# Kernel tuning notes

Hardware: AMD Instinct MI355X
Metric: run time of the kernel (lower is better)

Reference implementation:

```python
import jax, jax.numpy as jnp
import numpy as np

DIM = 384
B = 256
EPS = 1e-5


def _conv_replicate(x, W, pad):
    # x: [B,C,H,W], W: [O,I,kh,kw]; replicate (edge) padding then VALID conv
    x = jnp.pad(x, ((0, 0), (0, 0), (pad, pad), (pad, pad)), mode='edge')
    return jax.lax.conv_general_dilated(
        x, W, window_strides=(1, 1), padding='VALID',
        dimension_numbers=('NCHW', 'OIHW', 'NCHW'))


def _bn(x, g, b, m, v):
    scale = (g / jnp.sqrt(v + EPS))[None, :, None, None]
    return (x - m[None, :, None, None]) * scale + b[None, :, None, None]


def _clip_features(target, bbox):
    # target: [B, 576, C] -> vectorized per-sample crop + nearest resize to 12x12
    bb = bbox * 24.0
    x, y, w, h = bb[:, 0], bb[:, 1], bb[:, 2], bb[:, 3]
    l = (w + h) / 2
    l = jnp.sqrt((w + l) * (h + l))
    x_min = jnp.clip(jnp.ceil(x - l / 2), 0, 23).astype(jnp.int32)
    y_min = jnp.clip(jnp.ceil(y - l / 2), 0, 23).astype(jnp.int32)
    x_max = jnp.clip(jnp.trunc(x + l / 2), 0, 23).astype(jnp.int32)
    y_max = jnp.clip(jnp.trunc(y + l / 2), 0, 23).astype(jnp.int32)
    i12 = jnp.arange(12, dtype=jnp.int32)
    # nearest-neighbor source index: crop_start + floor(i * crop_size / 12)
    rows = y_min[:, None] + (i12[None, :] * (y_max - y_min)[:, None]) // 12  # [B,12]
    cols = x_min[:, None] + (i12[None, :] * (x_max - x_min)[:, None]) // 12  # [B,12]
    rows = jnp.clip(rows, 0, 23)
    cols = jnp.clip(cols, 0, 23)
    Bn, N, C = target.shape
    tflat = jnp.transpose(target, (0, 2, 1))  # [B, C, 576] (row-major 24x24)
    idx = rows[:, :, None] * 24 + cols[:, None, :]  # [B,12,12]
    idx = jnp.broadcast_to(idx.reshape(Bn, 1, 144), (Bn, C, 144))
    out = jnp.take_along_axis(tflat, idx, axis=2)  # [B, C, 144]
    return out.reshape(Bn, C, 12, 12)


def setup_inputs() -> dict:
    key = jax.random.key(0)
    ks = jax.random.split(key, 8)
    temp = jax.random.normal(ks[0], (B, 144, DIM), dtype=jnp.float32)
    target = jax.random.normal(ks[1], (B, 576, DIM), dtype=jnp.float32)
    u = jax.random.uniform(ks[2], (B, 4), dtype=jnp.float32)
    # centers in [0.3,0.7], sizes in [0.25,0.45] -> always a valid non-empty crop
    bbox = jnp.concatenate([0.3 + 0.4 * u[:, :2], 0.25 + 0.2 * u[:, 2:]], axis=1)
    W1 = jax.random.normal(ks[3], (DIM, DIM, 5, 5), dtype=jnp.float32) * 0.02
    W2 = jax.random.normal(ks[4], (DIM, DIM, 3, 3), dtype=jnp.float32) * 0.05
    g1 = jnp.ones((DIM,), jnp.float32)
    b1 = jnp.zeros((DIM,), jnp.float32)
    m1 = jax.random.normal(ks[5], (DIM,), dtype=jnp.float32) * 0.1
    v1 = jnp.ones((DIM,), jnp.float32)
    g2 = jnp.ones((DIM,), jnp.float32)
    b2 = jnp.zeros((DIM,), jnp.float32)
    m2 = jax.random.normal(ks[6], (DIM,), dtype=jnp.float32) * 0.1
    v2 = jnp.ones((DIM,), jnp.float32)
    return dict(temp=temp, target=target, bbox=bbox, W1=W1, g1=g1, b1=b1,
                m1=m1, v1=v1, W2=W2, g2=g2, b2=b2, m2=m2, v2=v2)


def reference(temp, target, bbox, W1, g1, b1, m1, v1, W2, g2, b2, m2, v2):
    ta = _clip_features(target, bbox)  # [B, C, 12, 12]
    h1 = jax.nn.leaky_relu(_bn(_conv_replicate(ta, W1, 2), g1, b1, m1, v1), 0.01)
    h2 = jax.nn.leaky_relu(_bn(_conv_replicate(h1, W2, 1), g2, b2, m2, v2), 0.01)
    Bn, N, C = temp.shape
    t = jnp.transpose(temp, (0, 2, 1)).reshape(Bn, C, 12, 12)
    out = (t + h2).reshape(Bn, C, 144)
    return jnp.transpose(out, (0, 2, 1))  # [B, 144, C]
```

## Files before the change

kernel.cpp:

```cpp
#include <hip/hip_runtime.h>
#include <math.h>

#define NBATCH 256
#define CDIM   384

typedef __attribute__((ext_vector_type(4))) float  f32x4;
typedef __attribute__((ext_vector_type(8))) __bf16 bf16x8;
typedef __attribute__((ext_vector_type(4))) __bf16 bf16x4;

__device__ __forceinline__ void load16(const void* g, void* l) {
    __builtin_amdgcn_global_load_lds(
        (const __attribute__((address_space(1))) void*)g,
        (__attribute__((address_space(3))) void*)l, 16, 0, 0);
}

__global__ __launch_bounds__(256) void gather_bf16(
    const float* __restrict__ target,
    const float* __restrict__ bbox,
    __bf16* __restrict__ ta)
{
    const int b = blockIdx.x, t = threadIdx.x;
    __shared__ int pos[144];

    if (t < 144) {
        const float bx0 = bbox[b * 4 + 0] * 24.f;
        const float by0 = bbox[b * 4 + 1] * 24.f;
        const float bw  = bbox[b * 4 + 2] * 24.f;
        const float bh  = bbox[b * 4 + 3] * 24.f;
        const float l0 = (bw + bh) * 0.5f;
        const float l  = sqrtf((bw + l0) * (bh + l0));
        const int xmin = (int)fminf(fmaxf(ceilf (bx0 - l * 0.5f), 0.f), 23.f);
        const int ymin = (int)fminf(fmaxf(ceilf (by0 - l * 0.5f), 0.f), 23.f);
        const int xmax = (int)fminf(fmaxf(truncf(bx0 + l * 0.5f), 0.f), 23.f);
        const int ymax = (int)fminf(fmaxf(truncf(by0 + l * 0.5f), 0.f), 23.f);
        const int i = t / 12, j = t % 12;
        int r = ymin + (i * (ymax - ymin)) / 12;
        int c = xmin + (j * (xmax - xmin)) / 12;
        r = min(max(r, 0), 23);
        c = min(max(c, 0), 23);
        pos[t] = r * 24 + c;
    }
    __syncthreads();

    const float* tb  = target + (size_t)b * 576 * 384;
    __bf16*      tab = ta     + (size_t)b * 144 * 384;
    for (int idx = t; idx < 144 * 96; idx += 256) {
        const int p = idx / 96, c4 = idx - p * 96;
        const float4 v = *(const float4*)&tb[(size_t)pos[p] * 384 + c4 * 4];
        bf16x4 o = { (__bf16)v.x, (__bf16)v.y, (__bf16)v.z, (__bf16)v.w };
        *(bf16x4*)&tab[(size_t)p * 384 + c4 * 4] = o;
    }
}

template <int TAPS>
__global__ __launch_bounds__(256) void prep_w(
    const float* __restrict__ W, __bf16* __restrict__ Wt)
{
    const int K = TAPS * 384;
    __shared__ float ws[TAPS * 384];
    const int oc = blockIdx.x;
    const float* src = W + (size_t)oc * K;
    for (int i = threadIdx.x; i < K; i += 256) ws[i] = src[i];
    __syncthreads();
    __bf16* dst = Wt + (size_t)oc * K;
    for (int i = threadIdx.x; i < K; i += 256) {
        const int tap = i / 384;
        const int ic  = i - tap * 384;
        dst[i] = (__bf16)ws[ic * TAPS + tap];
    }
}

template <int TAPS, int KW, int PAD, bool RESID>
__global__ __launch_bounds__(256, 2) void conv_mfma(
    const __bf16* __restrict__ A,
    const __bf16* __restrict__ Wt,
    const float* __restrict__ gg, const float* __restrict__ bb,
    const float* __restrict__ mm, const float* __restrict__ vv,
    const float* __restrict__ temp,
    void* __restrict__ outp)
{
    const int K  = TAPS * 384;
    const int IT = TAPS * 12;

    const int l    = blockIdx.x + 144 * blockIdx.y;
    const int work = (l & 7) * 54 + (l >> 3);
    const int wx   = work % 144, wy = work / 144;
    const int m0   = wx * 256;
    const int n0   = wy * 128;

    const int t  = threadIdx.x;
    const int lane  = t & 63, w = t >> 6;
    const int wm    = (w & 1) * 128, wn = (w >> 1) * 64;
    const int col16 = lane & 15,  quad = lane >> 4;

    __shared__ __bf16 As0[256 * 32], As1[256 * 32], As2[256 * 32];
    __shared__ __bf16 Bs0[128 * 32], Bs1[128 * 32], Bs2[128 * 32];

    const int r0   = t >> 2, slot = t & 3;
    const int kg   = slot ^ ((r0 >> 1) & 3);

    int yq[4], xq[4];
    const __bf16* Abq[4];
#pragma unroll
    for (int q = 0; q < 4; ++q) {
        const int mrow = m0 + r0 + 64 * q;
        const int b = mrow / 144, p = mrow - b * 144;
        yq[q] = p / 12;
        xq[q] = p - yq[q] * 12;
        Abq[q] = A + (size_t)b * 144 * 384 + kg * 8;
    }

    int offA[8], offB[4];
#pragma unroll
    for (int mi = 0; mi < 8; ++mi) {
        const int r = wm + mi * 16 + col16;
        offA[mi] = r * 32 + (quad ^ ((r >> 1) & 3)) * 8;
    }
#pragma unroll
    for (int ni = 0; ni < 4; ++ni) {
        const int r = wn + ni * 16 + col16;
        offB[ni] = r * 32 + (quad ^ ((r >> 1) & 3)) * 8;
    }

    f32x4 acc[8][4];
#pragma unroll
    for (int mi = 0; mi < 8; ++mi)
#pragma unroll
        for (int ni = 0; ni < 4; ++ni)
            acc[mi][ni] = (f32x4){0.f, 0.f, 0.f, 0.f};

    int jn = 0, tapn = 0, next = 0;
    const __bf16* aT[4];
#pragma unroll
    for (int q = 0; q < 4; ++q) {
        const int sy = min(max(yq[q] - PAD, 0), 11), sx = min(max(xq[q] - PAD, 0), 11);
        aT[q] = Abq[q] + (size_t)(sy * 12 + sx) * 384;
    }
    const __bf16* bT0 = Wt + (size_t)(n0 + r0)      * K + kg * 8;
    const __bf16* bT1 = Wt + (size_t)(n0 + r0 + 64) * K + kg * 8;

    auto issue = [&](__bf16* SA, __bf16* SB) {
#pragma unroll
        for (int q = 0; q < 4; ++q)
            load16(aT[q] + jn * 32, &SA[t * 8 + q * 2048]);
        load16(bT0 + jn * 32, &SB[t * 8]);
        load16(bT1 + jn * 32, &SB[t * 8 + 2048]);
    };
    auto advance = [&]() {
        if (++jn == 12) {
            jn = 0;
            ++tapn;
            if (tapn < TAPS) {
                const int ky = tapn / KW - PAD, kx = tapn % KW - PAD;
#pragma unroll
                for (int q = 0; q < 4; ++q) {
                    const int sy = min(max(yq[q] + ky, 0), 11);
                    const int sx = min(max(xq[q] + kx, 0), 11);
                    aT[q] = Abq[q] + (size_t)(sy * 12 + sx) * 384;
                }
                bT0 += 384;
                bT1 += 384;
            }
        }
    };
    auto step = [&](const __bf16* SA, const __bf16* SB,
                    __bf16* NA, __bf16* NB_, bool last) {
        if (last) asm volatile("s_waitcnt vmcnt(0)" ::: "memory");
        else      asm volatile("s_waitcnt vmcnt(6)" ::: "memory");
        __builtin_amdgcn_s_barrier();
        __builtin_amdgcn_sched_barrier(0);
        if (next < IT) { issue(NA, NB_); advance(); ++next; }
        bf16x8 av[8], bv[4];
#pragma unroll
        for (int ni = 0; ni < 4; ++ni) bv[ni] = *(const bf16x8*)&SB[offB[ni]];
#pragma unroll
        for (int mi = 0; mi < 8; ++mi) av[mi] = *(const bf16x8*)&SA[offA[mi]];
        __builtin_amdgcn_s_setprio(1);
#pragma unroll
        for (int mi = 0; mi < 8; ++mi)
#pragma unroll
            for (int ni = 0; ni < 4; ++ni)
                acc[mi][ni] = __builtin_amdgcn_mfma_f32_16x16x32_bf16(
                    av[mi], bv[ni], acc[mi][ni], 0, 0, 0);
        __builtin_amdgcn_s_setprio(0);
    };

    issue(As0, Bs0); advance(); ++next;
    issue(As1, Bs1); advance(); ++next;

    for (int it3 = 0; it3 < IT; it3 += 3) {
        step(As0, Bs0, As2, Bs2, it3 + 1 == IT);
        step(As1, Bs1, As0, Bs0, it3 + 2 == IT);
        step(As2, Bs2, As1, Bs1, it3 + 3 == IT);
    }

#pragma unroll
    for (int ni = 0; ni < 4; ++ni) {
        const int gn = n0 + wn + ni * 16 + col16;
        const float scale = gg[gn] * rsqrtf(vv[gn] + 1e-5f);
        const float shift = bb[gn] - mm[gn] * scale;
        if (!RESID) {
            __bf16* h1 = (__bf16*)outp;
#pragma unroll
            for (int mi = 0; mi < 8; ++mi) {
                const int gm = m0 + wm + mi * 16 + quad * 4;
#pragma unroll
                for (int r = 0; r < 4; ++r) {
                    float v = acc[mi][ni][r] * scale + shift;
                    v = (v >= 0.f) ? v : 0.01f * v;
                    h1[(size_t)(gm + r) * 384 + gn] = (__bf16)v;
                }
            }
        } else {
            float* outF = (float*)outp;
#pragma unroll
            for (int mi = 0; mi < 8; ++mi) {
                const int gm = m0 + wm + mi * 16 + quad * 4;
#pragma unroll
                for (int r = 0; r < 4; ++r) {
                    float v = acc[mi][ni][r] * scale + shift;
                    v = (v >= 0.f) ? v : 0.01f * v;
                    outF[(size_t)(gm + r) * 384 + gn] =
                        temp[(size_t)(gm + r) * 384 + gn] + v;
                }
            }
        }
    }
}

extern "C" void kernel_launch(void* const* d_in, const int* in_sizes, int n_in,
                              void* d_out, int out_size, void* d_ws, size_t ws_size,
                              hipStream_t stream) {
    const float* temp   = (const float*)d_in[0];
    const float* target = (const float*)d_in[1];
    const float* bbox   = (const float*)d_in[2];
    const float* W1     = (const float*)d_in[3];
    const float* g1     = (const float*)d_in[4];
    const float* b1     = (const float*)d_in[5];
    const float* m1     = (const float*)d_in[6];
    const float* v1     = (const float*)d_in[7];
    const float* W2     = (const float*)d_in[8];
    const float* g2     = (const float*)d_in[9];
    const float* b2     = (const float*)d_in[10];
    const float* m2     = (const float*)d_in[11];
    const float* v2     = (const float*)d_in[12];
    float* out = (float*)d_out;

    __bf16* ta  = (__bf16*)d_ws;
    __bf16* h1  = ta  + (size_t)NBATCH * 144 * CDIM;
    __bf16* Wt1 = h1  + (size_t)NBATCH * 144 * CDIM;
    __bf16* Wt2 = Wt1 + (size_t)CDIM * 25 * CDIM;

    prep_w<25><<<dim3(CDIM), dim3(256), 0, stream>>>(W1, Wt1);
    prep_w<9><<<dim3(CDIM), dim3(256), 0, stream>>>(W2, Wt2);
    gather_bf16<<<dim3(NBATCH), dim3(256), 0, stream>>>(target, bbox, ta);

    conv_mfma<25, 5, 2, false><<<dim3(144, 3), dim3(256), 0, stream>>>(
        ta, Wt1, g1, b1, m1, v1, nullptr, (void*)h1);
    conv_mfma<9, 3, 1, true><<<dim3(144, 3), dim3(256), 0, stream>>>(
        h1, Wt2, g2, b2, m2, v2, temp, (void*)out);
}
```

Baseline: 954.6 us.

## Load weight fragments directly to registers and reorder K loop channel-major

Weights are pre-laid out in MFMA-fragment order, so each thread loads its B operand straight from global memory into registers and the B tiles no longer pass through LDS. The K iteration order changes from tap-major to channel-chunk-major, and A addresses are recomputed per step instead of per tap. This removes B shared memory and its LDS reads. In exchange it adds register pressure from three in-flight B register buffers, uncoalesced-looking global loads shared redundantly across waves, and more per-step address arithmetic.

```diff
diff --git a/kernel.cpp b/kernel.cpp
--- a/kernel.cpp
+++ b/kernel.cpp
@@ -53,8 +53,8 @@
 }
 
 template <int TAPS>
-__global__ __launch_bounds__(256) void prep_w(
-    const float* __restrict__ W, __bf16* __restrict__ Wt)
+__global__ __launch_bounds__(256) void prep_w_frag(
+    const float* __restrict__ W, __bf16* __restrict__ Wf)
 {
     const int K = TAPS * 384;
     __shared__ float ws[TAPS * 384];
@@ -62,24 +62,24 @@
     const float* src = W + (size_t)oc * K;
     for (int i = threadIdx.x; i < K; i += 256) ws[i] = src[i];
     __syncthreads();
-    __bf16* dst = Wt + (size_t)oc * K;
     for (int i = threadIdx.x; i < K; i += 256) {
         const int tap = i / 384;
         const int ic  = i - tap * 384;
-        dst[i] = (__bf16)ws[ic * TAPS + tap];
+        const int jnn = ic >> 5, kk = ic & 31;
+        Wf[((size_t)(tap * 12 + jnn) * 384 + oc) * 32 + kk] =
+            (__bf16)ws[ic * TAPS + tap];
     }
 }
 
 template <int TAPS, int KW, int PAD, bool RESID>
 __global__ __launch_bounds__(256, 2) void conv_mfma(
     const __bf16* __restrict__ A,
-    const __bf16* __restrict__ Wt,
+    const __bf16* __restrict__ Wf,
     const float* __restrict__ gg, const float* __restrict__ bb,
     const float* __restrict__ mm, const float* __restrict__ vv,
     const float* __restrict__ temp,
     void* __restrict__ outp)
 {
-    const int K  = TAPS * 384;
     const int IT = TAPS * 12;
 
     const int l    = blockIdx.x + 144 * blockIdx.y;
@@ -94,7 +94,6 @@
     const int col16 = lane & 15,  quad = lane >> 4;
 
     __shared__ __bf16 As0[256 * 32], As1[256 * 32], As2[256 * 32];
-    __shared__ __bf16 Bs0[128 * 32], Bs1[128 * 32], Bs2[128 * 32];
 
     const int r0   = t >> 2, slot = t & 3;
     const int kg   = slot ^ ((r0 >> 1) & 3);
@@ -110,17 +109,17 @@
         Abq[q] = A + (size_t)b * 144 * 384 + kg * 8;
     }
 
-    int offA[8], offB[4];
+    int offA[8];
 #pragma unroll
     for (int mi = 0; mi < 8; ++mi) {
         const int r = wm + mi * 16 + col16;
         offA[mi] = r * 32 + (quad ^ ((r >> 1) & 3)) * 8;
     }
-#pragma unroll
-    for (int ni = 0; ni < 4; ++ni) {
-        const int r = wn + ni * 16 + col16;
-        offB[ni] = r * 32 + (quad ^ ((r >> 1) & 3)) * 8;
-    }
+    int loffB[4];
+#pragma unroll
+    for (int ni = 0; ni < 4; ++ni)
+        loffB[ni] = (wn + ni * 16 + col16) * 32 + quad * 8;
+    const __bf16* Bbase = Wf + (size_t)n0 * 32;
 
     f32x4 acc[8][4];
 #pragma unroll
@@ -129,50 +128,36 @@
         for (int ni = 0; ni < 4; ++ni)
             acc[mi][ni] = (f32x4){0.f, 0.f, 0.f, 0.f};
 
-    int jn = 0, tapn = 0, next = 0;
-    const __bf16* aT[4];
-#pragma unroll
-    for (int q = 0; q < 4; ++q) {
-        const int sy = min(max(yq[q] - PAD, 0), 11), sx = min(max(xq[q] - PAD, 0), 11);
-        aT[q] = Abq[q] + (size_t)(sy * 12 + sx) * 384;
-    }
-    const __bf16* bT0 = Wt + (size_t)(n0 + r0)      * K + kg * 8;
-    const __bf16* bT1 = Wt + (size_t)(n0 + r0 + 64) * K + kg * 8;
-
-    auto issue = [&](__bf16* SA, __bf16* SB) {
-#pragma unroll
-        for (int q = 0; q < 4; ++q)
-            load16(aT[q] + jn * 32, &SA[t * 8 + q * 2048]);
-        load16(bT0 + jn * 32, &SB[t * 8]);
-        load16(bT1 + jn * 32, &SB[t * 8 + 2048]);
+    int jn = 0, tap = 0, ky = -PAD, kx = -PAD, ksl = 0, next = 0;
+    auto advance = [&]() {
+        ++tap; ksl += 12; ++kx;
+        if (tap == TAPS)          { tap = 0; ++jn; ksl = jn; ky = -PAD; kx = -PAD; }
+        else if (kx == KW - PAD)  { kx = -PAD; ++ky; }
     };
-    auto advance = [&]() {
-        if (++jn == 12) {
-            jn = 0;
-            ++tapn;
-            if (tapn < TAPS) {
-                const int ky = tapn / KW - PAD, kx = tapn % KW - PAD;
-#pragma unroll
-                for (int q = 0; q < 4; ++q) {
-                    const int sy = min(max(yq[q] + ky, 0), 11);
-                    const int sx = min(max(xq[q] + kx, 0), 11);
-                    aT[q] = Abq[q] + (size_t)(sy * 12 + sx) * 384;
-                }
-                bT0 += 384;
-                bT1 += 384;
-            }
+
+    auto issue = [&](__bf16* SA, bf16x8* bvN) {
+#pragma unroll
+        for (int q = 0; q < 4; ++q) {
+            const int sy = min(max(yq[q] + ky, 0), 11);
+            const int sx = min(max(xq[q] + kx, 0), 11);
+            load16(Abq[q] + (size_t)(sy * 12 + sx) * 384 + jn * 32,
+                   &SA[t * 8 + q * 2048]);
         }
+        __builtin_amdgcn_sched_barrier(0);
+        const __bf16* Bk = Bbase + (size_t)ksl * (384 * 32);
+#pragma unroll
+        for (int ni = 0; ni < 4; ++ni)
+            bvN[ni] = *(const bf16x8*)(Bk + loffB[ni]);
     };
-    auto step = [&](const __bf16* SA, const __bf16* SB,
-                    __bf16* NA, __bf16* NB_, bool last) {
+
+    auto step = [&](const __bf16* SA, const bf16x8* bvC,
+                    __bf16* NA, bf16x8* bvN, bool last) {
         if (last) asm volatile("s_waitcnt vmcnt(0)" ::: "memory");
-        else      asm volatile("s_waitcnt vmcnt(6)" ::: "memory");
+        else      asm volatile("s_waitcnt vmcnt(8)" ::: "memory");
         __builtin_amdgcn_s_barrier();
         __builtin_amdgcn_sched_barrier(0);
-        if (next < IT) { issue(NA, NB_); advance(); ++next; }
-        bf16x8 av[8], bv[4];
-#pragma unroll
-        for (int ni = 0; ni < 4; ++ni) bv[ni] = *(const bf16x8*)&SB[offB[ni]];
+        if (next < IT) { issue(NA, bvN); advance(); ++next; }
+        bf16x8 av[8];
 #pragma unroll
         for (int mi = 0; mi < 8; ++mi) av[mi] = *(const bf16x8*)&SA[offA[mi]];
         __builtin_amdgcn_s_setprio(1);
@@ -181,17 +166,18 @@
 #pragma unroll
             for (int ni = 0; ni < 4; ++ni)
                 acc[mi][ni] = __builtin_amdgcn_mfma_f32_16x16x32_bf16(
-                    av[mi], bv[ni], acc[mi][ni], 0, 0, 0);
+                    av[mi], bvC[ni], acc[mi][ni], 0, 0, 0);
         __builtin_amdgcn_s_setprio(0);
     };
 
-    issue(As0, Bs0); advance(); ++next;
-    issue(As1, Bs1); advance(); ++next;
+    bf16x8 bv0[4], bv1[4], bv2[4];
+    issue(As0, bv0); __builtin_amdgcn_sched_barrier(0); advance(); ++next;
+    issue(As1, bv1); __builtin_amdgcn_sched_barrier(0); advance(); ++next;
 
     for (int it3 = 0; it3 < IT; it3 += 3) {
-        step(As0, Bs0, As2, Bs2, it3 + 1 == IT);
-        step(As1, Bs1, As0, Bs0, it3 + 2 == IT);
-        step(As2, Bs2, As1, Bs1, it3 + 3 == IT);
+        step(As0, bv0, As2, bv2, it3 + 1 == IT);
+        step(As1, bv1, As0, bv0, it3 + 2 == IT);
+        step(As2, bv2, As1, bv1, it3 + 3 == IT);
     }
 
 #pragma unroll
@@ -248,15 +234,15 @@
 
     __bf16* ta  = (__bf16*)d_ws;
     __bf16* h1  = ta  + (size_t)NBATCH * 144 * CDIM;
-    __bf16* Wt1 = h1  + (size_t)NBATCH * 144 * CDIM;
-    __bf16* Wt2 = Wt1 + (size_t)CDIM * 25 * CDIM;
-
-    prep_w<25><<<dim3(CDIM), dim3(256), 0, stream>>>(W1, Wt1);
-    prep_w<9><<<dim3(CDIM), dim3(256), 0, stream>>>(W2, Wt2);
+    __bf16* Wf1 = h1  + (size_t)NBATCH * 144 * CDIM;
+    __bf16* Wf2 = Wf1 + (size_t)CDIM * 25 * CDIM;
+
+    prep_w_frag<25><<<dim3(CDIM), dim3(256), 0, stream>>>(W1, Wf1);
+    prep_w_frag<9><<<dim3(CDIM), dim3(256), 0, stream>>>(W2, Wf2);
     gather_bf16<<<dim3(NBATCH), dim3(256), 0, stream>>>(target, bbox, ta);
 
     conv_mfma<25, 5, 2, false><<<dim3(144, 3), dim3(256), 0, stream>>>(
-        ta, Wt1, g1, b1, m1, v1, nullptr, (void*)h1);
+        ta, Wf1, g1, b1, m1, v1, nullptr, (void*)h1);
     conv_mfma<9, 3, 1, true><<<dim3(144, 3), dim3(256), 0, stream>>>(
-        h1, Wt2, g2, b2, m2, v2, temp, (void*)out);
-}
+        h1, Wf2, g2, b2, m2, v2, temp, (void*)out);
+}
```

New measurement: 1.842 ms. 1.93x slower.
